# Performance work log

Hardware: AMD Instinct MI355X
Metric: run time of the kernel (lower is better)

The kernel has to match this reference:

```python
import jax, jax.numpy as jnp
import numpy as np

IN_F = 4096
OUT_F = 4096
NNZ = 167772  # int(IN_F*OUT_F*0.01)
B, S = 4, 2048
ALPHA = 1.0  # self.alpha (privacy enabled)


def setup_inputs() -> dict:
    key = jax.random.key(0)
    k1, k2, k3, k4, k5 = jax.random.split(key, 5)
    x = jax.random.normal(k1, (B, S, IN_F), dtype=jnp.float32)
    # quantized-then-dequantized base weights stored in fp16
    base_weights = (jax.random.normal(k2, (OUT_F, IN_F), dtype=jnp.float32) * 0.02).astype(jnp.float16)
    # sparse outlier residual in COO form (equivalent to the module's CSR buffers)
    ortho_rows = jax.random.randint(k3, (NNZ,), 0, OUT_F, dtype=jnp.int32)
    ortho_cols = jax.random.randint(k4, (NNZ,), 0, IN_F, dtype=jnp.int32)
    ortho_vals = (jax.random.normal(k5, (NNZ,), dtype=jnp.float32) * 1e-3).astype(jnp.float16)
    return {"x": x, "base_weights": base_weights, "ortho_vals": ortho_vals,
            "ortho_rows": ortho_rows, "ortho_cols": ortho_cols}


def reference(x, base_weights, ortho_vals, ortho_rows, ortho_cols):
    orig_shape = x.shape
    orig_dtype = x.dtype
    x_flat = x.reshape(-1, IN_F)                                   # [N, in]
    # Base stream: fp16 GEMM, accumulated to fp32 (matches torch.mm on fp16 then .to(f32))
    out_base = jnp.matmul(x_flat.astype(jnp.float16), base_weights.T).astype(jnp.float32)  # [N, out]
    # Ortho stream: sparse CSR residual, computed in fp32 (vals upcast like the module)
    # Scatter the nnz outliers into a dense [out, in] matrix once, then a single GEMM
    # (same math as torch.sparse.mm over the CSR tensor, without per-chunk loops).
    w_ortho = jnp.zeros((OUT_F, IN_F), jnp.float32).at[ortho_rows, ortho_cols].add(
        ortho_vals.astype(jnp.float32))
    out_ortho = jnp.matmul(x_flat.astype(jnp.float32), w_ortho.T)  # [N, out]
    out_flat = out_base + ALPHA * out_ortho
    return out_flat.reshape(orig_shape[:-1] + (OUT_F,)).astype(orig_dtype)
```

## Files before the change

kernel.cpp:

```cpp
#include <hip/hip_runtime.h>
#include <stdint.h>

#define IN_F 4096
#define OUT_F 4096
#define NTOK 8192
#define NNZ_CNT 167772

typedef __attribute__((ext_vector_type(4))) float f32x4;
typedef __attribute__((ext_vector_type(8))) __bf16 bf16x8;
typedef __attribute__((ext_vector_type(8))) unsigned short u16x8;

__device__ __forceinline__ unsigned short f2bf(float f) {
  union { float f; unsigned int i; } u; u.f = f;
  unsigned int i = u.i;
  unsigned int r = (i + 0x7FFFu + ((i >> 16) & 1u)) >> 16;
  return (unsigned short)r;
}
__device__ __forceinline__ float bf2f(unsigned short h) {
  union { unsigned int i; float f; } u; u.i = ((unsigned int)h) << 16;
  return u.f;
}
__device__ __forceinline__ float sanitize(float f, float lim) {
  if (f >= -lim && f <= lim) return f;
  if (f > lim) return lim;
  if (f < -lim) return -lim;
  return 0.f;
}

__global__ void detect_dtype_kernel(const unsigned short* __restrict__ w, int* __restrict__ flag) {
  __shared__ int cnt;
  if (threadIdx.x == 0) cnt = 0;
  __syncthreads();
  int local = 0;
  for (int j = 0; j < 16; ++j) {
    unsigned short u = w[threadIdx.x * 16 + j];
    int e = (u >> 7) & 0xFF;
    if (u != 0 && e >= 107 && e <= 126) local++;
  }
  atomicAdd(&cnt, local);
  __syncthreads();
  if (threadIdx.x == 0) *flag = (cnt >= 3481) ? 0 : 1;
}

__global__ void combine_w_kernel(const void* __restrict__ bw, u16x8* __restrict__ wc,
                                 const int* __restrict__ flag, int n8) {
  const bool isf32 = (*flag != 0);
  int i = blockIdx.x * blockDim.x + threadIdx.x;
  int stride = gridDim.x * blockDim.x;
  for (; i < n8; i += stride) {
    u16x8 o;
    if (isf32) {
      const float4* s = (const float4*)bw + i * 2;
      float4 v0 = s[0], v1 = s[1];
      o[0] = f2bf(sanitize(v0.x, 1.f)); o[1] = f2bf(sanitize(v0.y, 1.f));
      o[2] = f2bf(sanitize(v0.z, 1.f)); o[3] = f2bf(sanitize(v0.w, 1.f));
      o[4] = f2bf(sanitize(v1.x, 1.f)); o[5] = f2bf(sanitize(v1.y, 1.f));
      o[6] = f2bf(sanitize(v1.z, 1.f)); o[7] = f2bf(sanitize(v1.w, 1.f));
    } else {
      u16x8 v = ((const u16x8*)bw)[i];
#pragma unroll
      for (int j = 0; j < 8; ++j) o[j] = f2bf(sanitize(bf2f(v[j]), 1.f));
    }
    wc[i] = o;
  }
}

__global__ void cvt_x_kernel(const float4* __restrict__ x, u16x8* __restrict__ xb, int n8) {
  int i = blockIdx.x * blockDim.x + threadIdx.x;
  int stride = gridDim.x * blockDim.x;
  for (; i < n8; i += stride) {
    float4 v0 = x[i * 2], v1 = x[i * 2 + 1];
    u16x8 o;
    o[0] = f2bf(sanitize(v0.x, 64.f)); o[1] = f2bf(sanitize(v0.y, 64.f));
    o[2] = f2bf(sanitize(v0.z, 64.f)); o[3] = f2bf(sanitize(v0.w, 64.f));
    o[4] = f2bf(sanitize(v1.x, 64.f)); o[5] = f2bf(sanitize(v1.y, 64.f));
    o[6] = f2bf(sanitize(v1.z, 64.f)); o[7] = f2bf(sanitize(v1.w, 64.f));
    xb[i] = o;
  }
}

__global__ void scatter_kernel(const void* __restrict__ vals,
                               const int* __restrict__ rows,
                               const int* __restrict__ cols,
                               unsigned short* __restrict__ W,
                               const int* __restrict__ flag) {
  int i = blockIdx.x * blockDim.x + threadIdx.x;
  if (i >= NNZ_CNT) return;
  int r = rows[i], c = cols[i];
  if ((unsigned)r >= OUT_F || (unsigned)c >= IN_F) return;
  float v = (*flag != 0) ? ((const float*)vals)[i] : bf2f(((const unsigned short*)vals)[i]);
  v = sanitize(v, 1.f);
  unsigned int* addr = (unsigned int*)(W + (size_t)r * IN_F + (c & ~1));
  bool hi = (c & 1);
  unsigned int old = *addr, assumed;
  do {
    assumed = old;
    unsigned short h = hi ? (unsigned short)(assumed >> 16) : (unsigned short)(assumed & 0xFFFFu);
    unsigned short nh = f2bf(bf2f(h) + v);
    unsigned int nw = hi ? ((assumed & 0x0000FFFFu) | ((unsigned int)nh << 16))
                         : ((assumed & 0xFFFF0000u) | (unsigned int)nh);
    old = atomicCAS(addr, assumed, nw);
  } while (old != assumed);
}

#define GLOAD16(g, l)                                                                  \
  __builtin_amdgcn_global_load_lds((const __attribute__((address_space(1))) void*)(g), \
                                   (__attribute__((address_space(3))) void*)(l), 16, 0, 0)

__global__ __launch_bounds__(512, 2) void gemm256_kernel(
    const unsigned short* __restrict__ Abf,
    const unsigned short* __restrict__ Bw,
    float* __restrict__ C) {
  __shared__ __align__(16) char lds[147456];
  const int t = threadIdx.x;
  const int l = t & 63;
  const int wv = t >> 6;
  const int wm = wv >> 2;
  const int wn = wv & 3;
  const int l15 = l & 15;

  const int nwg = gridDim.x;
  const int cpx = nwg >> 3;
  const int swz = (blockIdx.x & 7) * cpx + (blockIdx.x >> 3);
  const int bm = (swz >> 5) * 256;
  const int bn = (swz & 31) * 128;

  const int srow = t >> 3;
  const int scol = ((t & 7) ^ ((t >> 3) & 7)) * 8;
  const unsigned short* aSrc0 = Abf + (size_t)(bm + srow) * IN_F + scol;
  const unsigned short* bSrc0 = Bw + (size_t)(bn + srow) * IN_F + scol;
  char* ldsc = lds;

#define A_SRC(h, j, kt) (aSrc0 + ((((h)*128 + (j)*64) << 12) + ((kt) << 6)))
#define B_SRC(j, kt)    (bSrc0 + ((((j)*64) << 12) + ((kt) << 6)))
#define A_DST(h, j, b)  (ldsc + (b)*49152 + (h)*16384 + (j)*8192 + wv*1024)
#define B_DST(j, b)     (ldsc + (b)*49152 + 32768 + (j)*8192 + wv*1024)
#define STAGE_KT(kt, b) do {                       \
    GLOAD16(A_SRC(0, 0, kt), A_DST(0, 0, b));      \
    GLOAD16(A_SRC(0, 1, kt), A_DST(0, 1, b));      \
    GLOAD16(B_SRC(0, kt),    B_DST(0, b));         \
    GLOAD16(B_SRC(1, kt),    B_DST(1, b));         \
    GLOAD16(A_SRC(1, 0, kt), A_DST(1, 0, b));      \
    GLOAD16(A_SRC(1, 1, kt), A_DST(1, 1, b)); } while (0)

  const int u0 = (l >> 4) ^ (l & 7);
  const int u1 = u0 ^ 4;
  const int aBase = (wm * 128 + l15) * 8;
  const int bBase = 2048 + (wn * 32 + l15) * 8;
  const bf16x8* smp = (const bf16x8*)lds;

  f32x4 acc[8][2] = {};

  STAGE_KT(0, 0);
  STAGE_KT(1, 1);

  int cur = 0;
  for (int kt = 0; kt < 64; ++kt) {
    const int b2 = (cur >= 1) ? cur - 1 : 2;
    const int k2 = (kt + 2 < 64) ? kt + 2 : 63;
    const int cb16 = cur * 3072;
    bf16x8 af[4][2], bfr[2][2];

    asm volatile("s_waitcnt vmcnt(6)" ::: "memory");
    asm volatile("s_barrier" ::: "memory");
#pragma unroll
    for (int mi = 0; mi < 4; ++mi) {
      af[mi][0] = smp[cb16 + aBase + mi * 128 + u0];
      af[mi][1] = smp[cb16 + aBase + mi * 128 + u1];
    }
#pragma unroll
    for (int ni = 0; ni < 2; ++ni) {
      bfr[ni][0] = smp[cb16 + bBase + ni * 128 + u0];
      bfr[ni][1] = smp[cb16 + bBase + ni * 128 + u1];
    }
    GLOAD16(A_SRC(0, 0, k2), A_DST(0, 0, b2));
    GLOAD16(A_SRC(0, 1, k2), A_DST(0, 1, b2));
    GLOAD16(B_SRC(0, k2), B_DST(0, b2));
    asm volatile("s_barrier" ::: "memory");
    __builtin_amdgcn_s_setprio(1);
#pragma unroll
    for (int kk = 0; kk < 2; ++kk)
#pragma unroll
      for (int mi = 0; mi < 4; ++mi)
#pragma unroll
        for (int ni = 0; ni < 2; ++ni)
          acc[mi][ni] = __builtin_amdgcn_mfma_f32_16x16x32_bf16(
              af[mi][kk], bfr[ni][kk], acc[mi][ni], 0, 0, 0);
    __builtin_amdgcn_s_setprio(0);
    asm volatile("s_barrier" ::: "memory");

#pragma unroll
    for (int mi = 0; mi < 4; ++mi) {
      af[mi][0] = smp[cb16 + aBase + 512 + mi * 128 + u0];
      af[mi][1] = smp[cb16 + aBase + 512 + mi * 128 + u1];
    }
    GLOAD16(B_SRC(1, k2), B_DST(1, b2));
    GLOAD16(A_SRC(1, 0, k2), A_DST(1, 0, b2));
    GLOAD16(A_SRC(1, 1, k2), A_DST(1, 1, b2));
    asm volatile("s_barrier" ::: "memory");
    __builtin_amdgcn_s_setprio(1);
#pragma unroll
    for (int kk = 0; kk < 2; ++kk)
#pragma unroll
      for (int mi = 0; mi < 4; ++mi)
#pragma unroll
        for (int ni = 0; ni < 2; ++ni)
          acc[4 + mi][ni] = __builtin_amdgcn_mfma_f32_16x16x32_bf16(
              af[mi][kk], bfr[ni][kk], acc[4 + mi][ni], 0, 0, 0);
    __builtin_amdgcn_s_setprio(0);
    asm volatile("s_barrier" ::: "memory");

    cur = (cur < 2) ? cur + 1 : 0;
  }

#pragma unroll
  for (int mi = 0; mi < 8; ++mi) {
#pragma unroll
    for (int ni = 0; ni < 2; ++ni) {
      int row0 = bm + wm * 128 + mi * 16 + ((l >> 4) << 2);
      int col = bn + wn * 32 + ni * 16 + l15;
#pragma unroll
      for (int r = 0; r < 4; ++r)
        C[(size_t)(row0 + r) * OUT_F + col] = acc[mi][ni][r];
    }
  }
#undef A_SRC
#undef B_SRC
#undef A_DST
#undef B_DST
#undef STAGE_KT
}

__global__ __launch_bounds__(256, 3) void gemm_kernel(
    const float* __restrict__ Af, const unsigned short* __restrict__ Bw, float* __restrict__ C) {
  __shared__ bf16x8 smem[2048];
  const int tid = threadIdx.x;
  const int lane = tid & 63;
  const int wv = tid >> 6;
  const int bm = blockIdx.x * 128;
  const int bn = blockIdx.y * 128;
  const int srow = wv * 8 + (lane >> 3);
  const int scol = (lane & 7) * 8;
  const int wr = wv >> 1, wc = wv & 1;
  f32x4 acc[4][4] = {};
  const float* afp[4];
  const unsigned short* bptr[4];
#pragma unroll
  for (int q = 0; q < 4; ++q) {
    afp[q] = Af + (size_t)(bm + q * 32 + srow) * IN_F + scol;
    bptr[q] = Bw + (size_t)(bn + q * 32 + srow) * IN_F + scol;
  }
  char* smbase = (char*)smem;
  for (int k0 = 0; k0 < IN_F; k0 += 64) {
    __syncthreads();
#pragma unroll
    for (int q = 0; q < 4; ++q)
      GLOAD16(bptr[q] + k0, smbase + 16384 + q * 4096 + wv * 1024);
#pragma unroll
    for (int q = 0; q < 4; ++q) {
      const float* s = afp[q] + k0;
      float4 v0 = ((const float4*)s)[0];
      float4 v1 = ((const float4*)s)[1];
      u16x8 p;
      p[0] = f2bf(sanitize(v0.x, 64.f)); p[1] = f2bf(sanitize(v0.y, 64.f));
      p[2] = f2bf(sanitize(v0.z, 64.f)); p[3] = f2bf(sanitize(v0.w, 64.f));
      p[4] = f2bf(sanitize(v1.x, 64.f)); p[5] = f2bf(sanitize(v1.y, 64.f));
      p[6] = f2bf(sanitize(v1.z, 64.f)); p[7] = f2bf(sanitize(v1.w, 64.f));
      ((u16x8*)smem)[q * 256 + wv * 64 + lane] = p;
    }
    __syncthreads();
#pragma unroll
    for (int kk = 0; kk < 2; ++kk) {
      bf16x8 av[4], bv[4];
#pragma unroll
      for (int m = 0; m < 4; ++m)
        av[m] = smem[(wr * 64 + m * 16 + (lane & 15)) * 8 + kk * 4 + (lane >> 4)];
#pragma unroll
      for (int n = 0; n < 4; ++n)
        bv[n] = smem[1024 + (wc * 64 + n * 16 + (lane & 15)) * 8 + kk * 4 + (lane >> 4)];
#pragma unroll
      for (int m = 0; m < 4; ++m)
#pragma unroll
        for (int n = 0; n < 4; ++n)
          acc[m][n] = __builtin_amdgcn_mfma_f32_16x16x32_bf16(av[m], bv[n], acc[m][n], 0, 0, 0);
    }
  }
#pragma unroll
  for (int m = 0; m < 4; ++m)
#pragma unroll
    for (int n = 0; n < 4; ++n) {
      int row0 = bm + wr * 64 + m * 16 + ((lane >> 4) << 2);
      int col = bn + wc * 64 + n * 16 + (lane & 15);
#pragma unroll
      for (int r = 0; r < 4; ++r)
        C[(size_t)(row0 + r) * OUT_F + col] = acc[m][n][r];
    }
}

__global__ void naive_gemm_kernel(const float* __restrict__ x, const void* __restrict__ W,
                                  float* __restrict__ out, const int* __restrict__ flag) {
  const bool isf32 = (*flag != 0);
  int o = blockIdx.x * 256 + threadIdx.x;
  int t = blockIdx.y;
  const float* xr = x + (size_t)t * IN_F;
  float acc = 0.f;
  if (isf32) {
    const float* wr = (const float*)W + (size_t)o * IN_F;
    for (int k = 0; k < IN_F; ++k) acc += bf2f(f2bf(xr[k])) * bf2f(f2bf(sanitize(wr[k], 1.f)));
  } else {
    const unsigned short* wr = (const unsigned short*)W + (size_t)o * IN_F;
    for (int k = 0; k < IN_F; ++k) acc += bf2f(f2bf(xr[k])) * sanitize(bf2f(wr[k]), 1.f);
  }
  out[(size_t)t * OUT_F + o] = acc;
}
__global__ void naive_sparse_kernel(const float* __restrict__ x, const void* __restrict__ vals,
                                    const int* __restrict__ rows, const int* __restrict__ cols,
                                    float* __restrict__ out, const int* __restrict__ flag) {
  const bool isf32 = (*flag != 0);
  int t = blockIdx.x * 256 + threadIdx.x;
  if (t >= NTOK) return;
  const float* xr = x + (size_t)t * IN_F;
  float* orow = out + (size_t)t * OUT_F;
  for (int i = 0; i < NNZ_CNT; ++i) {
    int r = rows[i], c = cols[i];
    if ((unsigned)r >= OUT_F || (unsigned)c >= IN_F) continue;
    float v = isf32 ? ((const float*)vals)[i] : bf2f(((const unsigned short*)vals)[i]);
    orow[r] += sanitize(v, 1.f) * xr[c];
  }
}

extern "C" void kernel_launch(void* const* d_in, const int* in_sizes, int n_in,
                              void* d_out, int out_size, void* d_ws, size_t ws_size,
                              hipStream_t stream) {
  (void)out_size;
  const int NX = NTOK * IN_F, NW = OUT_F * IN_F;
  int ix = -1, ib = -1, qs[3], nq = 0;
  for (int i = 0; i < n_in; ++i) {
    if (in_sizes[i] == NX) ix = i;
    else if (in_sizes[i] == NW) ib = i;
    else if (in_sizes[i] == NNZ_CNT && nq < 3) qs[nq++] = i;
  }
  if (ix < 0 || ib < 0 || nq < 3) { ix = 0; ib = 1; qs[0] = 2; qs[1] = 3; qs[2] = 4; }
  const float* x = (const float*)d_in[ix];
  const void* bw = d_in[ib];
  const int* rows = (const int*)d_in[qs[1]];
  const void* vals;
  const int* cols;
  if (ix < ib) { vals = d_in[qs[0]]; cols = (const int*)d_in[qs[2]]; }
  else         { vals = d_in[qs[2]]; cols = (const int*)d_in[qs[0]]; }
  float* out = (float*)d_out;

  const size_t w_bytes = (size_t)OUT_F * IN_F * 2;
  const size_t xb_bytes = (size_t)NTOK * IN_F * 2;

  if (ws_size < w_bytes + 64) {
    int* flag = (int*)d_ws;
    hipLaunchKernelGGL(detect_dtype_kernel, dim3(1), dim3(256), 0, stream,
                       (const unsigned short*)bw, flag);
    hipLaunchKernelGGL(naive_gemm_kernel, dim3(OUT_F / 256, NTOK), dim3(256), 0, stream,
                       x, bw, out, flag);
    hipLaunchKernelGGL(naive_sparse_kernel, dim3((NTOK + 255) / 256), dim3(256), 0, stream,
                       x, vals, rows, cols, out, flag);
    return;
  }

  unsigned short* wcmb = (unsigned short*)d_ws;
  const bool big = ws_size >= w_bytes + xb_bytes + 4096;
  unsigned short* xb = (unsigned short*)((char*)d_ws + w_bytes);
  int* flag = (int*)((char*)d_ws + (big ? (w_bytes + xb_bytes) : w_bytes));

  hipLaunchKernelGGL(detect_dtype_kernel, dim3(1), dim3(256), 0, stream,
                     (const unsigned short*)bw, flag);
  hipLaunchKernelGGL(combine_w_kernel, dim3(2048), dim3(256), 0, stream,
                     bw, (u16x8*)wcmb, flag, NW / 8);
  hipLaunchKernelGGL(scatter_kernel, dim3((NNZ_CNT + 255) / 256), dim3(256), 0, stream,
                     vals, rows, cols, wcmb, flag);

  if (big) {
    hipLaunchKernelGGL(cvt_x_kernel, dim3(2048), dim3(256), 0, stream,
                       (const float4*)x, (u16x8*)xb, NX / 8);
    hipLaunchKernelGGL(gemm256_kernel, dim3((NTOK / 256) * (OUT_F / 128)), dim3(512), 0, stream,
                       xb, wcmb, out);
  } else {
    hipLaunchKernelGGL(gemm_kernel, dim3(NTOK / 128, OUT_F / 128), dim3(256), 0, stream,
                       x, wcmb, out);
  }
}
```

Measured before the change: 355.4 us.

## Enlarge GEMM tile to 256x256 with half-K double-buffered LDS staging

The main bf16 GEMM kernel moves from 256x128 tiles to 256x256 tiles, so each wave holds an 8x4 grid of accumulators instead of 8x2. The K=64 slice is now staged as two 32-wide halves in a double buffer rather than a triple buffer of full slices, with a new swizzle and a 512-block grid. The goal is more MFMA work per byte loaded into LDS and fewer global reloads of the A and B tiles. In exchange, register pressure roughly doubles on the accumulators, which could cut occupancy. There are also fewer workgroups, which may underfill the CUs.

```diff
diff --git a/kernel.cpp b/kernel.cpp
--- a/kernel.cpp
+++ b/kernel.cpp
@@ -111,7 +111,7 @@
     const unsigned short* __restrict__ Abf,
     const unsigned short* __restrict__ Bw,
     float* __restrict__ C) {
-  __shared__ __align__(16) char lds[147456];
+  __shared__ __align__(16) char lds[131072];
   const int t = threadIdx.x;
   const int l = t & 63;
   const int wv = t >> 6;
@@ -119,116 +119,110 @@
   const int wn = wv & 3;
   const int l15 = l & 15;
 
-  const int nwg = gridDim.x;
-  const int cpx = nwg >> 3;
-  const int swz = (blockIdx.x & 7) * cpx + (blockIdx.x >> 3);
-  const int bm = (swz >> 5) * 256;
-  const int bn = (swz & 31) * 128;
-
-  const int srow = t >> 3;
-  const int scol = ((t & 7) ^ ((t >> 3) & 7)) * 8;
-  const unsigned short* aSrc0 = Abf + (size_t)(bm + srow) * IN_F + scol;
-  const unsigned short* bSrc0 = Bw + (size_t)(bn + srow) * IN_F + scol;
-  char* ldsc = lds;
-
-#define A_SRC(h, j, kt) (aSrc0 + ((((h)*128 + (j)*64) << 12) + ((kt) << 6)))
-#define B_SRC(j, kt)    (bSrc0 + ((((j)*64) << 12) + ((kt) << 6)))
-#define A_DST(h, j, b)  (ldsc + (b)*49152 + (h)*16384 + (j)*8192 + wv*1024)
-#define B_DST(j, b)     (ldsc + (b)*49152 + 32768 + (j)*8192 + wv*1024)
-#define STAGE_KT(kt, b) do {                       \
-    GLOAD16(A_SRC(0, 0, kt), A_DST(0, 0, b));      \
-    GLOAD16(A_SRC(0, 1, kt), A_DST(0, 1, b));      \
-    GLOAD16(B_SRC(0, kt),    B_DST(0, b));         \
-    GLOAD16(B_SRC(1, kt),    B_DST(1, b));         \
-    GLOAD16(A_SRC(1, 0, kt), A_DST(1, 0, b));      \
-    GLOAD16(A_SRC(1, 1, kt), A_DST(1, 1, b)); } while (0)
-
-  const int u0 = (l >> 4) ^ (l & 7);
-  const int u1 = u0 ^ 4;
-  const int aBase = (wm * 128 + l15) * 8;
-  const int bBase = 2048 + (wn * 32 + l15) * 8;
+  const int swz = (blockIdx.x & 7) * 64 + (blockIdx.x >> 3);
+  const int bm = (swz >> 4) * 256;
+  const int bn = (swz & 15) * 256;
+
+  const int srow = t >> 2;
+  const int sunit = (t & 3) ^ ((t >> 3) & 3);
+  const unsigned short* aS0 = Abf + (size_t)(bm + srow) * IN_F + sunit * 8;
+  const unsigned short* aS1 = aS0 + (size_t)128 * IN_F;
+  const unsigned short* bS0 = Bw + (size_t)(bn + srow) * IN_F + sunit * 8;
+  const unsigned short* bS1 = bS0 + (size_t)128 * IN_F;
+  char* dstA = (char*)lds + wv * 1024;
+  char* dstB = (char*)lds + 32768 + wv * 1024;
+
+  const int u = (l >> 4) ^ ((l15 >> 1) & 3);
+  const int iA = (wm * 128 + l15) * 4 + u;
+  const int iB = 2048 + (wn * 64 + l15) * 4 + u;
   const bf16x8* smp = (const bf16x8*)lds;
 
-  f32x4 acc[8][2] = {};
-
-  STAGE_KT(0, 0);
-  STAGE_KT(1, 1);
-
-  int cur = 0;
+  f32x4 acc[8][4] = {};
+
+  GLOAD16(aS0 + 0, dstA + 0);          GLOAD16(aS1 + 0, dstA + 8192);
+  GLOAD16(bS0 + 0, dstB + 0);          GLOAD16(bS1 + 0, dstB + 8192);
+  GLOAD16(aS0 + 32, dstA + 16384);     GLOAD16(aS1 + 32, dstA + 16384 + 8192);
+  GLOAD16(bS0 + 32, dstB + 16384);     GLOAD16(bS1 + 32, dstB + 16384 + 8192);
+  GLOAD16(aS0 + 64, dstA + 65536);     GLOAD16(aS1 + 64, dstA + 65536 + 8192);
+  GLOAD16(bS0 + 64, dstB + 65536);     GLOAD16(bS1 + 64, dstB + 65536 + 8192);
+
   for (int kt = 0; kt < 64; ++kt) {
-    const int b2 = (cur >= 1) ? cur - 1 : 2;
-    const int k2 = (kt + 2 < 64) ? kt + 2 : 63;
-    const int cb16 = cur * 3072;
-    bf16x8 af[4][2], bfr[2][2];
-
-    asm volatile("s_waitcnt vmcnt(6)" ::: "memory");
+    const int c = kt & 1;
+    const int cU = c << 12;
+    const int s1 = ((kt + 1 < 64) ? (kt + 1) : 63) * 64 + 32;
+    const int s2 = ((kt + 2 < 64) ? (kt + 2) : 63) * 64;
+    const int d1 = (c ^ 1) * 65536 + 16384;
+    const int d2 = c * 65536;
+    bf16x8 av[4], bv[4];
+
+    asm volatile("s_waitcnt vmcnt(8) lgkmcnt(0)" ::: "memory");
     asm volatile("s_barrier" ::: "memory");
 #pragma unroll
-    for (int mi = 0; mi < 4; ++mi) {
-      af[mi][0] = smp[cb16 + aBase + mi * 128 + u0];
-      af[mi][1] = smp[cb16 + aBase + mi * 128 + u1];
-    }
-#pragma unroll
-    for (int ni = 0; ni < 2; ++ni) {
-      bfr[ni][0] = smp[cb16 + bBase + ni * 128 + u0];
-      bfr[ni][1] = smp[cb16 + bBase + ni * 128 + u1];
-    }
-    GLOAD16(A_SRC(0, 0, k2), A_DST(0, 0, b2));
-    GLOAD16(A_SRC(0, 1, k2), A_DST(0, 1, b2));
-    GLOAD16(B_SRC(0, k2), B_DST(0, b2));
+    for (int mi = 0; mi < 4; ++mi) av[mi] = smp[cU + iA + mi * 64];
+#pragma unroll
+    for (int ni = 0; ni < 4; ++ni) bv[ni] = smp[cU + iB + ni * 64];
+    GLOAD16(aS0 + s1, dstA + d1);
+    GLOAD16(aS1 + s1, dstA + d1 + 8192);
+    __builtin_amdgcn_s_setprio(1);
+#pragma unroll
+    for (int mi = 0; mi < 4; ++mi)
+#pragma unroll
+      for (int ni = 0; ni < 4; ++ni)
+        acc[mi][ni] = __builtin_amdgcn_mfma_f32_16x16x32_bf16(av[mi], bv[ni], acc[mi][ni], 0, 0, 0);
+    __builtin_amdgcn_s_setprio(0);
+
+#pragma unroll
+    for (int mi = 0; mi < 4; ++mi) av[mi] = smp[cU + iA + (mi + 4) * 64];
+    GLOAD16(bS0 + s1, dstB + d1);
+    GLOAD16(bS1 + s1, dstB + d1 + 8192);
+    __builtin_amdgcn_s_setprio(1);
+#pragma unroll
+    for (int mi = 0; mi < 4; ++mi)
+#pragma unroll
+      for (int ni = 0; ni < 4; ++ni)
+        acc[mi + 4][ni] = __builtin_amdgcn_mfma_f32_16x16x32_bf16(av[mi], bv[ni], acc[mi + 4][ni], 0, 0, 0);
+    __builtin_amdgcn_s_setprio(0);
+
+    asm volatile("s_waitcnt vmcnt(8) lgkmcnt(0)" ::: "memory");
     asm volatile("s_barrier" ::: "memory");
+#pragma unroll
+    for (int mi = 0; mi < 4; ++mi) av[mi] = smp[cU + 1024 + iA + mi * 64];
+#pragma unroll
+    for (int ni = 0; ni < 4; ++ni) bv[ni] = smp[cU + 1024 + iB + ni * 64];
+    GLOAD16(aS0 + s2, dstA + d2);
+    GLOAD16(aS1 + s2, dstA + d2 + 8192);
     __builtin_amdgcn_s_setprio(1);
 #pragma unroll
-    for (int kk = 0; kk < 2; ++kk)
-#pragma unroll
-      for (int mi = 0; mi < 4; ++mi)
-#pragma unroll
-        for (int ni = 0; ni < 2; ++ni)
-          acc[mi][ni] = __builtin_amdgcn_mfma_f32_16x16x32_bf16(
-              af[mi][kk], bfr[ni][kk], acc[mi][ni], 0, 0, 0);
+    for (int mi = 0; mi < 4; ++mi)
+#pragma unroll
+      for (int ni = 0; ni < 4; ++ni)
+        acc[mi][ni] = __builtin_amdgcn_mfma_f32_16x16x32_bf16(av[mi], bv[ni], acc[mi][ni], 0, 0, 0);
     __builtin_amdgcn_s_setprio(0);
-    asm volatile("s_barrier" ::: "memory");
-
-#pragma unroll
-    for (int mi = 0; mi < 4; ++mi) {
-      af[mi][0] = smp[cb16 + aBase + 512 + mi * 128 + u0];
-      af[mi][1] = smp[cb16 + aBase + 512 + mi * 128 + u1];
-    }
-    GLOAD16(B_SRC(1, k2), B_DST(1, b2));
-    GLOAD16(A_SRC(1, 0, k2), A_DST(1, 0, b2));
-    GLOAD16(A_SRC(1, 1, k2), A_DST(1, 1, b2));
-    asm volatile("s_barrier" ::: "memory");
+
+#pragma unroll
+    for (int mi = 0; mi < 4; ++mi) av[mi] = smp[cU + 1024 + iA + (mi + 4) * 64];
+    GLOAD16(bS0 + s2, dstB + d2);
+    GLOAD16(bS1 + s2, dstB + d2 + 8192);
     __builtin_amdgcn_s_setprio(1);
 #pragma unroll
-    for (int kk = 0; kk < 2; ++kk)
-#pragma unroll
-      for (int mi = 0; mi < 4; ++mi)
-#pragma unroll
-        for (int ni = 0; ni < 2; ++ni)
-          acc[4 + mi][ni] = __builtin_amdgcn_mfma_f32_16x16x32_bf16(
-              af[mi][kk], bfr[ni][kk], acc[4 + mi][ni], 0, 0, 0);
+    for (int mi = 0; mi < 4; ++mi)
+#pragma unroll
+      for (int ni = 0; ni < 4; ++ni)
+        acc[mi + 4][ni] = __builtin_amdgcn_mfma_f32_16x16x32_bf16(av[mi], bv[ni], acc[mi + 4][ni], 0, 0, 0);
     __builtin_amdgcn_s_setprio(0);
-    asm volatile("s_barrier" ::: "memory");
-
-    cur = (cur < 2) ? cur + 1 : 0;
   }
 
 #pragma unroll
   for (int mi = 0; mi < 8; ++mi) {
 #pragma unroll
-    for (int ni = 0; ni < 2; ++ni) {
+    for (int ni = 0; ni < 4; ++ni) {
       int row0 = bm + wm * 128 + mi * 16 + ((l >> 4) << 2);
-      int col = bn + wn * 32 + ni * 16 + l15;
+      int col = bn + wn * 64 + ni * 16 + l15;
 #pragma unroll
       for (int r = 0; r < 4; ++r)
         C[(size_t)(row0 + r) * OUT_F + col] = acc[mi][ni][r];
     }
   }
-#undef A_SRC
-#undef B_SRC
-#undef A_DST
-#undef B_DST
-#undef STAGE_KT
 }
 
 __global__ __launch_bounds__(256, 3) void gemm_kernel(
@@ -379,7 +373,7 @@
   if (big) {
     hipLaunchKernelGGL(cvt_x_kernel, dim3(2048), dim3(256), 0, stream,
                        (const float4*)x, (u16x8*)xb, NX / 8);
-    hipLaunchKernelGGL(gemm256_kernel, dim3((NTOK / 256) * (OUT_F / 128)), dim3(512), 0, stream,
+    hipLaunchKernelGGL(gemm256_kernel, dim3((NTOK / 256) * (OUT_F / 256)), dim3(512), 0, stream,
                        xb, wcmb, out);
   } else {
     hipLaunchKernelGGL(gemm_kernel, dim3(NTOK / 128, OUT_F / 128), dim3(256), 0, stream,
```

Result: faster. 307.0 us (-13.6%).
